# Optimization experiments

Hardware: AMD Instinct MI355X
Metric: run time of the kernel (lower is better)

Reference implementation:

```python
import jax, jax.numpy as jnp
import numpy as np

INPUT_DIM = 512
EMBED_DIM = 64
B, S = 4, 4096


def setup_inputs() -> dict:
    key = jax.random.key(0)
    ks = jax.random.split(key, 9)
    scale = 1.0 / np.sqrt(INPUT_DIM)
    return {
        "q": jax.random.normal(ks[0], (B, S, INPUT_DIM), dtype=jnp.float32),
        "k": jax.random.normal(ks[1], (B, S, INPUT_DIM), dtype=jnp.float32),
        "v": jax.random.normal(ks[2], (B, S, INPUT_DIM), dtype=jnp.float32),
        "Wq": jax.random.uniform(ks[3], (INPUT_DIM, EMBED_DIM), jnp.float32, -scale, scale),
        "bq": jax.random.uniform(ks[4], (EMBED_DIM,), jnp.float32, -scale, scale),
        "Wk": jax.random.uniform(ks[5], (INPUT_DIM, EMBED_DIM), jnp.float32, -scale, scale),
        "bk": jax.random.uniform(ks[6], (EMBED_DIM,), jnp.float32, -scale, scale),
        "Wv": jax.random.uniform(ks[7], (INPUT_DIM, EMBED_DIM), jnp.float32, -scale, scale),
        "bv": jax.random.uniform(ks[8], (EMBED_DIM,), jnp.float32, -scale, scale),
    }


def reference(q, k, v, Wq, bq, Wk, bk, Wv, bv):
    # Linear projections (torch Linear: x @ W^T + b; here W stored as [in, out])
    Q = q @ Wq + bq  # [B, S, E]
    K = k @ Wk + bk  # [B, S, E]
    V = v @ Wv + bv  # [B, S, E]
    d_k = K.shape[-1]
    scores = jnp.einsum("bqe,bke->bqk", Q, K) / jnp.sqrt(jnp.float32(d_k))  # [B, S, S]
    attn = jax.nn.softmax(scores, axis=-1)
    return jnp.einsum("bqk,bke->bqe", attn, V)  # [B, S, E]
```

## Files before the change

### kernel.cpp

```cpp
#include <hip/hip_runtime.h>
#include <math.h>

#define S_ 4096
#define C_SCALE 0.18033688011112042f
#define KSPLIT 8

typedef __attribute__((ext_vector_type(4))) float  floatx4;
typedef __attribute__((ext_vector_type(4))) short  short4_t;
typedef __attribute__((ext_vector_type(8))) short  short8_t;
typedef __attribute__((ext_vector_type(2))) unsigned int uintx2;
typedef __attribute__((ext_vector_type(4))) unsigned int uintx4;

__device__ __forceinline__ short f2bf(float f) {
  unsigned u = __builtin_bit_cast(unsigned, f);
  u += 0x7FFFu + ((u >> 16) & 1u);
  return (short)(u >> 16);
}
__device__ __forceinline__ unsigned pack2(float lo, float hi) {
  unsigned a = __builtin_bit_cast(unsigned, lo) + 0x8000u;
  unsigned b = __builtin_bit_cast(unsigned, hi) + 0x8000u;
  return __builtin_amdgcn_perm(b, a, 0x07060302u);
}
__device__ __forceinline__ unsigned packt(float lo, float hi) {
  return __builtin_amdgcn_perm(__builtin_bit_cast(unsigned, hi),
                               __builtin_bit_cast(unsigned, lo), 0x07060302u);
}
__device__ __forceinline__ float bf2f(short s) {
  return __builtin_bit_cast(float, (unsigned)((unsigned short)s) << 16);
}
__device__ __forceinline__ void dma16(const void* g, void* l) {
  __builtin_amdgcn_global_load_lds(
      (const __attribute__((address_space(1))) void*)g,
      (__attribute__((address_space(3))) void*)l, 16, 0, 0);
}

__global__ __launch_bounds__(256) void prep_w(const float* __restrict__ Wq,
                                              const float* __restrict__ Wk,
                                              const float* __restrict__ Wv,
                                              short* __restrict__ Wt) {
  __shared__ float T[64 * 65];
  int m = blockIdx.x >> 3, kt = blockIdx.x & 7, tid = threadIdx.x;
  const float* W = (m == 0) ? Wq : (m == 1) ? Wk : Wv;
  float sc = (m == 0) ? C_SCALE : 1.0f;
#pragma unroll
  for (int i = 0; i < 16; i++) {
    int e = i * 256 + tid;
    int k = e >> 6, n = e & 63;
    T[k * 65 + n] = W[(kt * 64 + k) * 64 + n];
  }
  __syncthreads();
#pragma unroll
  for (int i = 0; i < 16; i++) {
    int e = i * 256 + tid;
    int n = e >> 6, k = e & 63;
    Wt[m * 32768 + n * 512 + kt * 64 + k] = f2bf(T[k * 65 + n] * sc);
  }
}

__global__ __launch_bounds__(256, 3) void proj_kernel(
    const float* __restrict__ qin, const float* __restrict__ kin,
    const float* __restrict__ vin, const float* __restrict__ bq,
    const float* __restrict__ bk, const float* __restrict__ bv,
    const short* __restrict__ Wt, short* __restrict__ Qp,
    short* __restrict__ Kp, short* __restrict__ Vt) {
  __shared__ short A_lds[2][64 * 64];
  __shared__ short W_lds[2][64 * 64];

  int tid = threadIdx.x;
  int m = blockIdx.x >> 8;
  int r0 = (blockIdx.x & 255) * 64;
  int wid = tid >> 6, lane = tid & 63, l15 = lane & 15, quad = lane >> 4;

  const float* in = (m == 0) ? qin : (m == 1) ? kin : vin;
  const short* Wm = Wt + m * 32768;

  int sr = tid >> 3, sc = tid & 7;
  int sphys = ((sc ^ (sr & 7)) * 8);

  floatx4 ar[2][4];
  auto loadA = [&](int kc, int p) {
    const float* pA = in + (size_t)(r0 + sr) * 512 + kc * 64 + sc * 8;
    ar[p][0] = *(const floatx4*)pA;
    ar[p][1] = *(const floatx4*)(pA + 4);
    const float* p2 = pA + 32 * 512;
    ar[p][2] = *(const floatx4*)p2;
    ar[p][3] = *(const floatx4*)(p2 + 4);
  };
  auto dmaW = [&](int kc, int buf) {
#pragma unroll
    for (int j = 0; j < 2; j++) {
      int slot = wid * 128 + j * 64 + lane;
      int r = slot >> 3, c = slot & 7;
      int gc = (c ^ (r & 7)) * 8;
      dma16(Wm + r * 512 + kc * 64 + gc, (void*)&W_lds[buf][(wid * 2 + j) * 512]);
    }
  };
  auto packStoreA = [&](int p, int buf) {
    uintx4 w0 = {pack2(ar[p][0][0], ar[p][0][1]), pack2(ar[p][0][2], ar[p][0][3]),
                 pack2(ar[p][1][0], ar[p][1][1]), pack2(ar[p][1][2], ar[p][1][3])};
    uintx4 w1 = {pack2(ar[p][2][0], ar[p][2][1]), pack2(ar[p][2][2], ar[p][2][3]),
                 pack2(ar[p][3][0], ar[p][3][1]), pack2(ar[p][3][2], ar[p][3][3])};
    *(short8_t*)(&A_lds[buf][sr * 64 + sphys]) = __builtin_bit_cast(short8_t, w0);
    *(short8_t*)(&A_lds[buf][(sr + 32) * 64 + sphys]) = __builtin_bit_cast(short8_t, w1);
  };

  floatx4 acc[4];
#pragma unroll
  for (int nb = 0; nb < 4; nb++) acc[nb] = (floatx4){0.f, 0.f, 0.f, 0.f};

  loadA(0, 0);
  loadA(1, 1);
  dmaW(0, 0);
#pragma unroll
  for (int kc = 0; kc < 8; kc++) {
    packStoreA(kc & 1, kc & 1);
    __syncthreads();
    if (kc < 7) dmaW(kc + 1, (kc + 1) & 1);
    if (kc < 6) loadA(kc + 2, kc & 1);
    int arow = wid * 16 + l15;
    int akey = arow & 7, wkey = l15 & 7;
#pragma unroll
    for (int h = 0; h < 2; h++) {
      short8_t af =
          *(const short8_t*)(&A_lds[kc & 1][arow * 64 + ((h * 4 + quad) ^ akey) * 8]);
#pragma unroll
      for (int nb = 0; nb < 4; nb++) {
        short8_t wf = *(const short8_t*)(&W_lds[kc & 1][(nb * 16 + l15) * 64 +
                                                        ((h * 4 + quad) ^ wkey) * 8]);
        acc[nb] = __builtin_amdgcn_mfma_f32_16x16x32_bf16(af, wf, acc[nb], 0, 0, 0);
      }
    }
  }

  const float* bias = (m == 0) ? bq : (m == 1) ? bk : bv;
  float bsc = (m == 0) ? C_SCALE : 1.0f;
  if (m < 2) {
    short* out = (m == 0) ? Qp : Kp;
#pragma unroll
    for (int nb = 0; nb < 4; nb++) {
      float bv_ = bias[nb * 16 + l15] * bsc;
#pragma unroll
      for (int r = 0; r < 4; r++)
        out[(size_t)(r0 + wid * 16 + quad * 4 + r) * 64 + nb * 16 + l15] =
            f2bf(acc[nb][r] + bv_);
    }
  } else {
    int bb = r0 >> 12;
    int s0 = (r0 & 4095) + wid * 16 + quad * 4;
#pragma unroll
    for (int nb = 0; nb < 4; nb++) {
      float bv_ = bias[nb * 16 + l15];
      short4_t pk = {f2bf(acc[nb][0] + bv_), f2bf(acc[nb][1] + bv_),
                     f2bf(acc[nb][2] + bv_), f2bf(acc[nb][3] + bv_)};
      *(short4_t*)(Vt + (size_t)bb * 262144 + (nb * 16 + l15) * 4096 + s0) = pk;
    }
  }
}

__global__ __launch_bounds__(256, 2) void attn_kernel(
    const short* __restrict__ Qp, const short* __restrict__ Kp,
    const short* __restrict__ Vt, short* __restrict__ Po,
    float* __restrict__ Lp) {
  __shared__ short K_lds[2][64 * 64];
  __shared__ short V_lds[2][64 * 64];
  __shared__ short P_lds[4][64 * 64];

  int tid = threadIdx.x;
  int ks = blockIdx.x >> 6, b = (blockIdx.x >> 4) & 3, qt = blockIdx.x & 15;
  int wid = tid >> 6, lane = tid & 63, l15 = lane & 15, quad = lane >> 4;
  int key = l15 & 7;

  const short* Qb = Qp + (size_t)b * (S_ * 64);
  const short* Kb = Kp + (size_t)b * (S_ * 64);
  const short* Vb = Vt + (size_t)b * (64 * S_);

  int q0 = qt * 256 + wid * 64;

  short8_t qf[4][2];
#pragma unroll
  for (int qs = 0; qs < 4; qs++)
#pragma unroll
    for (int h = 0; h < 2; h++)
      qf[qs][h] = *(const short8_t*)(Qb + (q0 + qs * 16 + l15) * 64 + h * 32 + quad * 8);

  floatx4 o[4][4];
#pragma unroll
  for (int qs = 0; qs < 4; qs++)
#pragma unroll
    for (int eb = 0; eb < 4; eb++) o[qs][eb] = (floatx4){0.f, 0.f, 0.f, 0.f};
  float l_acc[4] = {0.f, 0.f, 0.f, 0.f};
  short* Pw = &P_lds[wid][0];
  int ks_base = ks * 512;

  auto stage = [&](int t, int buf) {
    int ks0 = ks_base + t * 64;
#pragma unroll
    for (int j = 0; j < 2; j++) {
      int slot = wid * 128 + j * 64 + lane;
      int r = slot >> 3, c = slot & 7;
      int gc = (c ^ (r & 7)) * 8;
      dma16(Kb + (ks0 + r) * 64 + gc, (void*)&K_lds[buf][(wid * 2 + j) * 512]);
      dma16(Vb + (size_t)r * 4096 + ks0 + gc, (void*)&V_lds[buf][(wid * 2 + j) * 512]);
    }
  };

  stage(0, 0);
  for (int t = 0; t < 8; t++) {
    __syncthreads();
    if (t < 7) stage(t + 1, (t + 1) & 1);
    const short* Kt = K_lds[t & 1];
    const short* Vl = V_lds[t & 1];

#pragma unroll
    for (int jh = 0; jh < 2; jh++) {
      short8_t kA[4];
#pragma unroll
      for (int jb = 0; jb < 2; jb++)
#pragma unroll
        for (int eh = 0; eh < 2; eh++)
          kA[jb * 2 + eh] = *(const short8_t*)(
              Kt + (jh * 32 + jb * 16 + l15) * 64 + ((eh * 4 + quad) ^ key) * 8);

#pragma unroll
      for (int qs = 0; qs < 4; qs++) {
        floatx4 z = (floatx4){0.f, 0.f, 0.f, 0.f};
        floatx4 s0 = __builtin_amdgcn_mfma_f32_16x16x32_bf16(kA[0], qf[qs][0], z, 0, 0, 0);
        s0 = __builtin_amdgcn_mfma_f32_16x16x32_bf16(kA[1], qf[qs][1], s0, 0, 0, 0);
        floatx4 s1 = __builtin_amdgcn_mfma_f32_16x16x32_bf16(kA[2], qf[qs][0], z, 0, 0, 0);
        s1 = __builtin_amdgcn_mfma_f32_16x16x32_bf16(kA[3], qf[qs][1], s1, 0, 0, 0);
        float e00 = __builtin_amdgcn_exp2f(s0[0]), e01 = __builtin_amdgcn_exp2f(s0[1]);
        float e02 = __builtin_amdgcn_exp2f(s0[2]), e03 = __builtin_amdgcn_exp2f(s0[3]);
        float e10 = __builtin_amdgcn_exp2f(s1[0]), e11 = __builtin_amdgcn_exp2f(s1[1]);
        float e12 = __builtin_amdgcn_exp2f(s1[2]), e13 = __builtin_amdgcn_exp2f(s1[3]);
        l_acc[qs] += ((e00 + e01) + (e02 + e03)) + ((e10 + e11) + (e12 + e13));
        int row = (qs * 16 + l15) * 64;
        uintx2 w0 = {packt(e00, e01), packt(e02, e03)};
        uintx2 w1 = {packt(e10, e11), packt(e12, e13)};
        *(uintx2*)(Pw + row + ((jh * 4 + 0 + (quad >> 1)) ^ key) * 8 + (quad & 1) * 4) = w0;
        *(uintx2*)(Pw + row + ((jh * 4 + 2 + (quad >> 1)) ^ key) * 8 + (quad & 1) * 4) = w1;
      }

      short8_t pf[4];
#pragma unroll
      for (int qs = 0; qs < 4; qs++)
        pf[qs] = *(const short8_t*)(Pw + (qs * 16 + l15) * 64 +
                                    ((jh * 4 + quad) ^ key) * 8);
      __builtin_amdgcn_s_setprio(1);
#pragma unroll
      for (int eb = 0; eb < 4; eb++) {
        short8_t vf = *(const short8_t*)(Vl + (eb * 16 + l15) * 64 +
                                         ((jh * 4 + quad) ^ key) * 8);
#pragma unroll
        for (int qs = 0; qs < 4; qs++)
          o[qs][eb] = __builtin_amdgcn_mfma_f32_16x16x32_bf16(pf[qs], vf, o[qs][eb], 0, 0, 0);
      }
      __builtin_amdgcn_s_setprio(0);
    }
  }

#pragma unroll
  for (int qs = 0; qs < 4; qs++) {
    float l = l_acc[qs];
    l += __shfl_xor(l, 16, 64);
    l += __shfl_xor(l, 32, 64);
    int grow_base = b * 4096 + q0 + qs * 16;
    short* Pb = Po + ((size_t)ks * 16384 + grow_base) * 64;
#pragma unroll
    for (int eb = 0; eb < 4; eb++)
#pragma unroll
      for (int r = 0; r < 4; r++)
        Pb[(size_t)(quad * 4 + r) * 64 + eb * 16 + l15] = f2bf(o[qs][eb][r]);
    if (quad == 0) Lp[ks * 16384 + grow_base + l15] = l;
  }
}

__global__ __launch_bounds__(256) void combine_kernel(
    const short* __restrict__ Po, const float* __restrict__ Lp,
    float* __restrict__ out) {
  int gid = blockIdx.x * 256 + threadIdx.x;
  int grow = gid >> 3, e0 = (gid & 7) * 8;
  float s[8];
#pragma unroll
  for (int i = 0; i < 8; i++) s[i] = 0.f;
  float l = 0.f;
#pragma unroll
  for (int ks = 0; ks < KSPLIT; ks++) {
    short8_t p = *(const short8_t*)(Po + ((size_t)ks * 16384 + grow) * 64 + e0);
#pragma unroll
    for (int i = 0; i < 8; i++) s[i] += bf2f(p[i]);
    l += Lp[ks * 16384 + grow];
  }
  float inv = 1.0f / l;
  floatx4 o0 = {s[0] * inv, s[1] * inv, s[2] * inv, s[3] * inv};
  floatx4 o1 = {s[4] * inv, s[5] * inv, s[6] * inv, s[7] * inv};
  *(floatx4*)(out + (size_t)grow * 64 + e0) = o0;
  *(floatx4*)(out + (size_t)grow * 64 + e0 + 4) = o1;
}

extern "C" void kernel_launch(void* const* d_in, const int* in_sizes, int n_in,
                              void* d_out, int out_size, void* d_ws, size_t ws_size,
                              hipStream_t stream) {
  const float* q = (const float*)d_in[0];
  const float* k = (const float*)d_in[1];
  const float* v = (const float*)d_in[2];
  const float* Wq = (const float*)d_in[3];
  const float* bq = (const float*)d_in[4];
  const float* Wk = (const float*)d_in[5];
  const float* bk = (const float*)d_in[6];
  const float* Wv = (const float*)d_in[7];
  const float* bv = (const float*)d_in[8];

  char* ws = (char*)d_ws;
  short* Qp = (short*)(ws);
  short* Kp = (short*)(ws + (1u << 21));
  short* Vt = (short*)(ws + (2u << 21));
  short* Wt = (short*)(ws + (3u << 21));
  short* Po = (short*)(ws + (4u << 21));
  float* Lp = (float*)(ws + (13u << 21));

  prep_w<<<24, 256, 0, stream>>>(Wq, Wk, Wv, Wt);
  proj_kernel<<<768, 256, 0, stream>>>(q, k, v, bq, bk, bv, Wt, Qp, Kp, Vt);
  attn_kernel<<<512, 256, 0, stream>>>(Qp, Kp, Vt, Po, Lp);
  combine_kernel<<<512, 256, 0, stream>>>(Po, Lp, (float*)d_out);
}
```

Measured before the change: 165.2 us.

## Reshape P into MFMA operand layout with permlane swaps instead of LDS round-trip

Removes the per-wave P staging buffer in shared memory. The softmax probabilities are rearranged into the B-operand layout in registers using permlane16/permlane32 swaps. To keep the result correct, the V projection now writes V transposed with a permuted key ordering that matches the new P column order. This removes LDS writes and reads plus their latency from the inner loop and frees 32KB of LDS, at the cost of a few cross-lane permute instructions and a less coalesced V store.

```diff
diff --git a/kernel.cpp b/kernel.cpp
--- a/kernel.cpp
+++ b/kernel.cpp
@@ -146,13 +146,17 @@
     }
   } else {
     int bb = r0 >> 12;
-    int s0 = (r0 & 4095) + wid * 16 + quad * 4;
+    int sb = (r0 & 4095) + (wid >> 1) * 32 + (wid & 1) * 16 + quad * 2;
 #pragma unroll
     for (int nb = 0; nb < 4; nb++) {
       float bv_ = bias[nb * 16 + l15];
-      short4_t pk = {f2bf(acc[nb][0] + bv_), f2bf(acc[nb][1] + bv_),
-                     f2bf(acc[nb][2] + bv_), f2bf(acc[nb][3] + bv_)};
-      *(short4_t*)(Vt + (size_t)bb * 262144 + (nb * 16 + l15) * 4096 + s0) = pk;
+      unsigned lo = (unsigned)(unsigned short)f2bf(acc[nb][0] + bv_) |
+                    ((unsigned)(unsigned short)f2bf(acc[nb][1] + bv_) << 16);
+      unsigned hi = (unsigned)(unsigned short)f2bf(acc[nb][2] + bv_) |
+                    ((unsigned)(unsigned short)f2bf(acc[nb][3] + bv_) << 16);
+      short* pV = Vt + (size_t)bb * 262144 + (nb * 16 + l15) * 4096 + sb;
+      *(unsigned*)pV = lo;
+      *(unsigned*)(pV + 8) = hi;
     }
   }
 }
@@ -163,7 +167,6 @@
     float* __restrict__ Lp) {
   __shared__ short K_lds[2][64 * 64];
   __shared__ short V_lds[2][64 * 64];
-  __shared__ short P_lds[4][64 * 64];
 
   int tid = threadIdx.x;
   int ks = blockIdx.x >> 6, b = (blockIdx.x >> 4) & 3, qt = blockIdx.x & 15;
@@ -189,7 +192,6 @@
 #pragma unroll
     for (int eb = 0; eb < 4; eb++) o[qs][eb] = (floatx4){0.f, 0.f, 0.f, 0.f};
   float l_acc[4] = {0.f, 0.f, 0.f, 0.f};
-  short* Pw = &P_lds[wid][0];
   int ks_base = ks * 512;
 
   auto stage = [&](int t, int buf) {
@@ -221,6 +223,7 @@
           kA[jb * 2 + eh] = *(const short8_t*)(
               Kt + (jh * 32 + jb * 16 + l15) * 64 + ((eh * 4 + quad) ^ key) * 8);
 
+      short8_t pf[4];
 #pragma unroll
       for (int qs = 0; qs < 4; qs++) {
         floatx4 z = (floatx4){0.f, 0.f, 0.f, 0.f};
@@ -233,18 +236,16 @@
         float e10 = __builtin_amdgcn_exp2f(s1[0]), e11 = __builtin_amdgcn_exp2f(s1[1]);
         float e12 = __builtin_amdgcn_exp2f(s1[2]), e13 = __builtin_amdgcn_exp2f(s1[3]);
         l_acc[qs] += ((e00 + e01) + (e02 + e03)) + ((e10 + e11) + (e12 + e13));
-        int row = (qs * 16 + l15) * 64;
-        uintx2 w0 = {packt(e00, e01), packt(e02, e03)};
-        uintx2 w1 = {packt(e10, e11), packt(e12, e13)};
-        *(uintx2*)(Pw + row + ((jh * 4 + 0 + (quad >> 1)) ^ key) * 8 + (quad & 1) * 4) = w0;
-        *(uintx2*)(Pw + row + ((jh * 4 + 2 + (quad >> 1)) ^ key) * 8 + (quad & 1) * 4) = w1;
+        unsigned d0 = packt(e00, e01), d1 = packt(e02, e03);
+        unsigned d2 = packt(e10, e11), d3 = packt(e12, e13);
+        uintx2 A0 = __builtin_amdgcn_permlane16_swap(d0, d1, false, false);
+        uintx2 A2 = __builtin_amdgcn_permlane16_swap(d2, d3, false, false);
+        uintx2 B0 = __builtin_amdgcn_permlane32_swap(A0[0], A2[0], false, false);
+        uintx2 B1 = __builtin_amdgcn_permlane32_swap(A0[1], A2[1], false, false);
+        uintx4 pw = {B0[0], B1[0], B0[1], B1[1]};
+        pf[qs] = __builtin_bit_cast(short8_t, pw);
       }
 
-      short8_t pf[4];
-#pragma unroll
-      for (int qs = 0; qs < 4; qs++)
-        pf[qs] = *(const short8_t*)(Pw + (qs * 16 + l15) * 64 +
-                                    ((jh * 4 + quad) ^ key) * 8);
       __builtin_amdgcn_s_setprio(1);
 #pragma unroll
       for (int eb = 0; eb < 4; eb++) {
```

After: 167.5 us. About the same (+1.4%).
